# Kernel tuning notes

Hardware: AMD Instinct MI355X
Metric: run time of the kernel (lower is better)

The kernel has to match this reference:

```python
import jax, jax.numpy as jnp
import numpy as np

MASK_PENALTY = 1e15  # matches the TF module's additive mask constant


def setup_inputs() -> dict:
    key = jax.random.key(0)
    k1, k2, k3, k4, k5 = jax.random.split(key, 5)
    B, S, E, DK, DV = 4, 2048, 1024, 128, 128
    inputs = jax.random.normal(k1, (B, S, E), dtype=jnp.float32)
    mask = jax.random.randint(k2, (B, S, S), 0, 2, dtype=jnp.int32)
    # Dense kernels (glorot-ish scale)
    Wq = jax.random.normal(k3, (E, DK), dtype=jnp.float32) / np.float32(np.sqrt(E))
    Wk = jax.random.normal(k4, (E, DK), dtype=jnp.float32) / np.float32(np.sqrt(E))
    Wv = jax.random.normal(k5, (E, DV), dtype=jnp.float32) / np.float32(np.sqrt(E))
    return {"inputs": inputs, "mask": mask, "Wq": Wq, "Wk": Wk, "Wv": Wv}


def reference(inputs, mask, Wq, Wk, Wv):
    # q, k, v projections (no bias)
    q = jnp.einsum("bse,ed->bsd", inputs, Wq)  # [B,S,DK]
    k = jnp.einsum("bse,ed->bsd", inputs, Wk)  # [B,S,DK]
    v = jnp.einsum("bse,ed->bsd", inputs, Wv)  # [B,S,DV]
    dim_k = Wq.shape[-1]
    scale = jnp.asarray(1.0 / np.sqrt(dim_k), dtype=q.dtype)
    dot_p = jnp.einsum("bqd,bkd->bqk", q, k) * scale  # [B,S,S]
    dot_p = dot_p - MASK_PENALTY * mask.astype(dot_p.dtype)
    softm = jax.nn.softmax(dot_p, axis=-1)
    return jnp.einsum("bqk,bkd->bqd", softm, v)  # [B,S,DV]
```

## Files before the change

### kernel.cpp

```cpp
#include <hip/hip_runtime.h>
#include <stdint.h>


#define SEQ   2048
#define EDIM  1024
#define DDIM  128
#define QSCALE 0.08838834764831845f

typedef unsigned short u16;
typedef unsigned int   u32;
using short8 = __attribute__((ext_vector_type(8))) short;
using f32x4  = __attribute__((ext_vector_type(4))) float;
using int4v  = __attribute__((ext_vector_type(4))) int;

__device__ __forceinline__ u16 f2bf(float x) {
    uint32_t u = __float_as_uint(x);
    return (u16)((u + 0x7fffu + ((u >> 16) & 1u)) >> 16);
}

__device__ __forceinline__ void gld16(const void* gsrc, void* lds_dst) {
    __builtin_amdgcn_global_load_lds(
        (const __attribute__((address_space(1))) uint32_t*)(uintptr_t)gsrc,
        (__attribute__((address_space(3))) uint32_t*)(uint32_t)(uintptr_t)lds_dst,
        16, 0, 0);
}

__global__ __launch_bounds__(256) void prep_kernel(
    const int* __restrict__ mask,
    const float* __restrict__ Wq, const float* __restrict__ Wk, const float* __restrict__ Wv,
    u32* __restrict__ Mbits, u16* __restrict__ Wt)
{
    __shared__ u32 nib32[2048];
    __shared__ u16 tl[64][65];
    const int bx = blockIdx.x;
    const int tid = threadIdx.x;
    if (bx < 2048) {
        const int* src = mask + (size_t)bx * 8192;
#pragma unroll
        for (int it = 0; it < 8; ++it) {
            const int idx = it * 256 + tid;
            const int4v v = *(const int4v*)(src + idx * 4);
            const u32 nb = (v[0] != 0 ? 1u : 0u) | (v[1] != 0 ? 2u : 0u)
                         | (v[2] != 0 ? 4u : 0u) | (v[3] != 0 ? 8u : 0u);
            nib32[(idx & 7) * 256 + ((idx >> 3) ^ ((idx & 7) << 2))] = nb;
        }
        __syncthreads();
        u32 word = 0;
#pragma unroll
        for (int j = 0; j < 8; ++j)
            word |= (nib32[j * 256 + (tid ^ (j << 2))] & 0xFu) << (4 * j);
        Mbits[bx * 256 + tid] = word;
    } else {
        const int t = bx - 2048;
        const int wsel = t >> 5;
        const int tile = t & 31;
        const int k0 = (tile >> 1) * 64;
        const int n0 = (tile & 1) * 64;
        const float* W = (wsel == 0) ? Wq : ((wsel == 1) ? Wk : Wv);
#pragma unroll
        for (int it = 0; it < 16; ++it) {
            const int idx = it * 256 + tid;
            const int r = idx >> 6, c = idx & 63;
            tl[c][r] = f2bf(W[(size_t)(k0 + r) * DDIM + n0 + c]);
        }
        __syncthreads();
        u16* Wtp = Wt + (size_t)wsel * DDIM * EDIM;
#pragma unroll
        for (int it = 0; it < 16; ++it) {
            const int idx = it * 256 + tid;
            const int r = idx >> 6, c = idx & 63;
            Wtp[(size_t)(n0 + r) * EDIM + k0 + c] = tl[r][c];
        }
    }
}

__global__ __launch_bounds__(256, 3) void proj_kernel(
    const float* __restrict__ Ain, const u16* __restrict__ Wtb,
    u16* __restrict__ Qb, u16* __restrict__ Kb, u16* __restrict__ Vtb)
{
    __shared__ __align__(16) uint8_t smem[20480];
    const int tid = threadIdx.x;
    const int w = tid >> 6, lane = tid & 63;
    const int lq = lane & 15, lg = lane >> 4;

    const int bid = blockIdx.x;
    const int wg = (bid & 7) * 96 + (bid >> 3);
    const int wm = wg % 3;
    const int m0 = (wg / 3) * 32;
    const u16* Wt = Wtb + (size_t)wm * DDIM * EDIM;

    f32x4 acc[2][2] = {};

#pragma unroll 1
    for (int kt = 0; kt < 16; ++kt) {
        const int k0 = kt * 64;
#pragma unroll
        for (int i = 0; i < 4; ++i) {
            const int G = i * 256 + tid;
            const int n = G >> 3, c = G & 7;
            gld16(Wt + (size_t)n * EDIM + k0 + ((c ^ (n & 7)) << 3),
                  smem + 4096 + i * 4096 + w * 1024);
        }
        {
            const int row = tid >> 3, c = tid & 7;
            const float* s2 = Ain + (size_t)(m0 + row) * EDIM + k0 + ((c ^ (row & 7)) << 3);
            const f32x4 a0 = *(const f32x4*)s2;
            const f32x4 a1 = *(const f32x4*)(s2 + 4);
            short8 v;
            v[0] = (short)f2bf(a0[0]); v[1] = (short)f2bf(a0[1]);
            v[2] = (short)f2bf(a0[2]); v[3] = (short)f2bf(a0[3]);
            v[4] = (short)f2bf(a1[0]); v[5] = (short)f2bf(a1[1]);
            v[6] = (short)f2bf(a1[2]); v[7] = (short)f2bf(a1[3]);
            *(short8*)(smem + row * 128 + (c << 4)) = v;
        }
        __syncthreads();
#pragma unroll
        for (int ks = 0; ks < 2; ++ks) {
            short8 af[2], bfv[2];
#pragma unroll
            for (int mf = 0; mf < 2; ++mf) {
                const int arow = mf * 16 + lq;
                af[mf] = *(const short8*)(smem + arow * 128 + ((((ks << 2) + lg) ^ (arow & 7)) << 4));
            }
#pragma unroll
            for (int nf = 0; nf < 2; ++nf) {
                const int brow = w * 32 + nf * 16 + lq;
                bfv[nf] = *(const short8*)(smem + 4096 + brow * 128 + ((((ks << 2) + lg) ^ (brow & 7)) << 4));
            }
#pragma unroll
            for (int mf = 0; mf < 2; ++mf)
#pragma unroll
                for (int nf = 0; nf < 2; ++nf)
                    acc[mf][nf] = __builtin_amdgcn_mfma_f32_16x16x32_bf16(af[mf], bfv[nf], acc[mf][nf], 0, 0, 0);
        }
        __syncthreads();
    }

    const float osc = (wm == 0) ? QSCALE : 1.0f;
    if (wm < 2) {
#pragma unroll
        for (int mf = 0; mf < 2; ++mf)
#pragma unroll
            for (int nf = 0; nf < 2; ++nf)
#pragma unroll
                for (int rr = 0; rr < 4; ++rr) {
                    const int row = mf * 16 + lg * 4 + rr;
                    const int col = w * 32 + nf * 16 + lq;
                    *(u16*)(smem + row * 256 + (((col >> 3) ^ (row & 7)) << 4) + ((col & 7) << 1))
                        = f2bf(acc[mf][nf][rr] * osc);
                }
        __syncthreads();
        u16* dst = (wm == 0 ? Qb : Kb) + (size_t)m0 * 128;
#pragma unroll
        for (int i = 0; i < 2; ++i) {
            const int j = i * 256 + tid;
            const int row = j >> 4, c = j & 15;
            *(short8*)(dst + (size_t)row * 128 + c * 8)
                = *(const short8*)(smem + row * 256 + ((c ^ (row & 7)) << 4));
        }
    } else {
#pragma unroll
        for (int mf = 0; mf < 2; ++mf)
#pragma unroll
            for (int nf = 0; nf < 2; ++nf)
#pragma unroll
                for (int rr = 0; rr < 4; ++rr) {
                    const int sl = mf * 16 + lg * 4 + rr;
                    const int d  = w * 32 + nf * 16 + lq;
                    *(u16*)(smem + d * 64 + (((sl >> 3) ^ (d & 3)) << 4) + ((sl & 7) << 1))
                        = f2bf(acc[mf][nf][rr]);
                }
        __syncthreads();
        const int b = m0 >> 11, s0b = m0 & 2047;
        u16* dst = Vtb + (size_t)b * DDIM * SEQ;
#pragma unroll
        for (int i = 0; i < 2; ++i) {
            const int j = i * 256 + tid;
            const int dd = j >> 2, c = j & 3;
            *(short8*)(dst + (size_t)dd * SEQ + s0b + c * 8)
                = *(const short8*)(smem + dd * 64 + ((c ^ (dd & 3)) << 4));
        }
    }
}

__global__ __launch_bounds__(512, 1) void flash_kernel(
    const u32* __restrict__ Mb,
    const u16* __restrict__ Qb, const u16* __restrict__ Kb, const u16* __restrict__ Vtb,
    float* __restrict__ out)
{
    __shared__ __align__(16) uint8_t smem[139264];
    __shared__ float ml_m[2][4][16], ml_l[2][4][16], recipL[32];

    const int tid = threadIdx.x;
    const int w = tid >> 6, lane = tid & 63;
    const int qi = w >> 2, ki = w & 3;
    const int lq = lane & 15, lg = lane >> 4;

    const int bid = blockIdx.x;
    const int qt = (bid & 7) * 32 + (bid >> 3);
    const int b = qt >> 6;
    const int q0 = (qt & 63) << 5;
    const size_t qrow0 = (size_t)b * SEQ + q0;

    const u16* Qp = Qb + (qrow0 + qi * 16) * 128;
    const u16* Kp = Kb + (size_t)b * SEQ * 128;
    const u16* Vp = Vtb + (size_t)b * DDIM * SEQ;
    const u32* mrp = Mb + (qrow0 + qi * 16 + lq) * 64 + ki * 16;

    short8 qf[4];
#pragma unroll
    for (int ks = 0; ks < 4; ++ks)
        qf[ks] = *(const short8*)(Qp + (size_t)lq * 128 + ks * 32 + lg * 8);

    f32x4 acc[8] = {};
    float m = -1e30f, l = 0.0f;

    uint8_t* kvb0 = smem + ki * 32768;
    uint8_t* pbase = smem + 131072 + w * 1024;

    auto stage = [&](uint8_t* kvb, int kv0) {
        if (qi == 0) {
#pragma unroll
            for (int i = 0; i < 8; ++i) {
                const int G = i * 64 + lane;
                const int row = G >> 4, c = G & 15;
                gld16(Kp + (size_t)(kv0 + row) * 128 + ((c ^ (row & 7)) << 3),
                      kvb + i * 1024);
            }
        } else {
#pragma unroll
            for (int i = 0; i < 8; ++i) {
                const int G = i * 64 + lane;
                const int dd = G >> 2, c = G & 3;
                gld16(Vp + (size_t)dd * SEQ + kv0 + ((c ^ ((dd ^ (dd >> 2)) & 3)) << 3),
                      kvb + 8192 + i * 1024);
            }
        }
    };

    stage(kvb0, ki * 512);
    u32 mw = mrp[0];
    asm volatile("s_waitcnt vmcnt(0)" ::: "memory");
    __builtin_amdgcn_s_barrier();

#pragma unroll 1
    for (int t = 0; t < 16; ++t) {
        uint8_t* kvb = kvb0 + (t & 1) * 16384;
        if (t < 15) stage(kvb0 + ((t + 1) & 1) * 16384, ki * 512 + (t + 1) * 32);
        const u32 mwn = mrp[(t < 15) ? t + 1 : 15];
        __builtin_amdgcn_sched_barrier(0);

        f32x4 sacc[2] = {};
        __builtin_amdgcn_s_setprio(1);
#pragma unroll
        for (int ks = 0; ks < 4; ++ks)
#pragma unroll
            for (int nf = 0; nf < 2; ++nf) {
                const int krow = nf * 16 + lq;
                const short8 kf = *(const short8*)(kvb + krow * 256 + ((((ks << 2) + lg) ^ (krow & 7)) << 4));
                sacc[nf] = __builtin_amdgcn_mfma_f32_16x16x32_bf16(kf, qf[ks], sacc[nf], 0, 0, 0);
            }
        __builtin_amdgcn_s_setprio(0);

        float sv[2][4];
#pragma unroll
        for (int nf = 0; nf < 2; ++nf)
#pragma unroll
            for (int r = 0; r < 4; ++r)
                sv[nf][r] = sacc[nf][r] + (((mw >> (nf * 16 + lg * 4 + r)) & 1u) ? -1e15f : 0.0f);
        float tm = sv[0][0];
#pragma unroll
        for (int nf = 0; nf < 2; ++nf)
#pragma unroll
            for (int r = 0; r < 4; ++r) tm = fmaxf(tm, sv[nf][r]);
        tm = fmaxf(tm, __shfl_xor(tm, 16));
        tm = fmaxf(tm, __shfl_xor(tm, 32));
        if (!__all(tm <= m + 8.0f)) {
            const float mnew = fmaxf(m, tm);
            const float sf = __expf(m - mnew);
            m = mnew;
            l *= sf;
#pragma unroll
            for (int df = 0; df < 8; ++df) acc[df] *= sf;
        }
        float p[2][4];
        float rs = 0.0f;
#pragma unroll
        for (int nf = 0; nf < 2; ++nf)
#pragma unroll
            for (int r = 0; r < 4; ++r) { p[nf][r] = __expf(sv[nf][r] - m); rs += p[nf][r]; }
        rs += __shfl_xor(rs, 16);
        rs += __shfl_xor(rs, 32);
        l += rs;
        mw = mwn;

#pragma unroll
        for (int nf = 0; nf < 2; ++nf)
#pragma unroll
            for (int h = 0; h < 2; ++h) {
                u32 pk;
                asm("v_cvt_pk_bf16_f32 %0, %1, %2" : "=v"(pk) : "v"(p[nf][2 * h]), "v"(p[nf][2 * h + 1]));
                const int kv = nf * 16 + lg * 4 + 2 * h;
                *(u32*)(pbase + lq * 64 + (((kv >> 3) ^ (lq & 3)) << 4) + ((kv << 1) & 15)) = pk;
            }
        const short8 pf = *(const short8*)(pbase + lq * 64 + ((lg ^ (lq & 3)) << 4));

        __builtin_amdgcn_s_setprio(1);
#pragma unroll
        for (int df = 0; df < 8; ++df) {
            const int dd = df * 16 + lq;
            const short8 vf = *(const short8*)(kvb + 8192 + dd * 64 + ((lg ^ ((dd ^ (dd >> 2)) & 3)) << 4));
            acc[df] = __builtin_amdgcn_mfma_f32_16x16x32_bf16(vf, pf, acc[df], 0, 0, 0);
        }
        __builtin_amdgcn_s_setprio(0);

        asm volatile("s_waitcnt vmcnt(0)" ::: "memory");
        __builtin_amdgcn_s_barrier();
    }

    if (lg == 0) { ml_m[qi][ki][lq] = m; ml_l[qi][ki][lq] = l; }
    __syncthreads();
    {
        const float m0v = ml_m[qi][0][lq], m1v = ml_m[qi][1][lq];
        const float m2v = ml_m[qi][2][lq], m3v = ml_m[qi][3][lq];
        const float mm = fmaxf(fmaxf(m0v, m1v), fmaxf(m2v, m3v));
        const float Lg = ml_l[qi][0][lq] * __expf(m0v - mm) + ml_l[qi][1][lq] * __expf(m1v - mm)
                       + ml_l[qi][2][lq] * __expf(m2v - mm) + ml_l[qi][3][lq] * __expf(m3v - mm);
        if (ki == 0 && lg == 0) recipL[qi * 16 + lq] = 1.0f / Lg;
        const float s = __expf(m - mm);
        float* Ol = (float*)smem;
        float* dstq = Ol + ((size_t)(qi * 4 + ki) * 16 + lq) * 132;
#pragma unroll
        for (int df = 0; df < 8; ++df) {
            const f32x4 vsc = acc[df] * s;
            *(f32x4*)(dstq + df * 16 + lg * 4) = vsc;
        }
    }
    __syncthreads();
    {
        const float* Ol = (const float*)smem;
        const int row = tid >> 4, c0 = (tid & 15) * 8;
        const int rqi = row >> 4, rq = row & 15;
        const float rl = recipL[row];
        f32x4 s0 = {}, s1 = {};
#pragma unroll
        for (int kk = 0; kk < 4; ++kk) {
            const float* p2 = Ol + ((size_t)(rqi * 4 + kk) * 16 + rq) * 132 + c0;
            s0 += *(const f32x4*)p2;
            s1 += *(const f32x4*)(p2 + 4);
        }
        s0 *= rl; s1 *= rl;
        float* op = out + (qrow0 + row) * 128 + c0;
        *(f32x4*)op = s0;
        *(f32x4*)(op + 4) = s1;
    }
}

extern "C" void kernel_launch(void* const* d_in, const int* in_sizes, int n_in,
                              void* d_out, int out_size, void* d_ws, size_t ws_size,
                              hipStream_t stream) {
    (void)in_sizes; (void)n_in; (void)out_size; (void)ws_size;
    const float* inputs = (const float*)d_in[0];
    const int*   mask   = (const int*)d_in[1];
    const float* Wq     = (const float*)d_in[2];
    const float* Wk     = (const float*)d_in[3];
    const float* Wv     = (const float*)d_in[4];
    float* out = (float*)d_out;

    uint8_t* ws = (uint8_t*)d_ws;
    u16* Wtb   = (u16*)ws;
    u16* Qb    = (u16*)(ws + 786432);
    u16* Kb    = (u16*)(ws + 2883584);
    u16* Vtb   = (u16*)(ws + 4980736);
    u32* Mbits = (u32*)(ws + 7077888);

    hipLaunchKernelGGL(prep_kernel, dim3(2144), dim3(256), 0, stream, mask, Wq, Wk, Wv, Mbits, Wtb);
    hipLaunchKernelGGL(proj_kernel, dim3(768), dim3(256), 0, stream, inputs, Wtb, Qb, Kb, Vtb);
    hipLaunchKernelGGL(flash_kernel, dim3(256), dim3(512), 0, stream, Mbits, Qb, Kb, Vtb, out);
}
```

Measured before the change: 170.3 us.

## Fuse mask bitpacking into flash kernel, merge QKV projection, use exp2

Mask bit-packing moves out of the prep kernel and into the flash kernel, which reads its own int32 mask rows into LDS bits. This removes a separate pass that wrote and then re-read a packed mask. The projection kernel now computes Q, K and V together in one 512-thread block per 32 rows with double-buffered LDS staging, so the input tile is loaded once instead of three times. Softmax switches to raw v_exp_f32 with log2e folded into the Q scale, and the rescale threshold is raised. Risks include mask-load latency at the start of the flash kernel and the higher skip threshold affecting precision.

```diff
diff --git a/kernel.cpp b/kernel.cpp
--- a/kernel.cpp
+++ b/kernel.cpp
@@ -5,17 +5,21 @@
 #define SEQ   2048
 #define EDIM  1024
 #define DDIM  128
-#define QSCALE 0.08838834764831845f
+#define QS2   0.1275174329f
 
 typedef unsigned short u16;
 typedef unsigned int   u32;
 using short8 = __attribute__((ext_vector_type(8))) short;
 using f32x4  = __attribute__((ext_vector_type(4))) float;
 using int4v  = __attribute__((ext_vector_type(4))) int;
+using u32x2  = __attribute__((ext_vector_type(2))) unsigned int;
 
 __device__ __forceinline__ u16 f2bf(float x) {
     uint32_t u = __float_as_uint(x);
     return (u16)((u + 0x7fffu + ((u >> 16) & 1u)) >> 16);
+}
+__device__ __forceinline__ float ex2(float x) {
+    float r; asm("v_exp_f32 %0, %1" : "=v"(r) : "v"(x)); return r;
 }
 
 __device__ __forceinline__ void gld16(const void* gsrc, void* lds_dst) {
@@ -26,169 +30,136 @@
 }
 
 __global__ __launch_bounds__(256) void prep_kernel(
-    const int* __restrict__ mask,
     const float* __restrict__ Wq, const float* __restrict__ Wk, const float* __restrict__ Wv,
-    u32* __restrict__ Mbits, u16* __restrict__ Wt)
+    u16* __restrict__ Wt)
 {
-    __shared__ u32 nib32[2048];
     __shared__ u16 tl[64][65];
-    const int bx = blockIdx.x;
+    const int t = blockIdx.x;
     const int tid = threadIdx.x;
-    if (bx < 2048) {
-        const int* src = mask + (size_t)bx * 8192;
-#pragma unroll
-        for (int it = 0; it < 8; ++it) {
-            const int idx = it * 256 + tid;
-            const int4v v = *(const int4v*)(src + idx * 4);
-            const u32 nb = (v[0] != 0 ? 1u : 0u) | (v[1] != 0 ? 2u : 0u)
-                         | (v[2] != 0 ? 4u : 0u) | (v[3] != 0 ? 8u : 0u);
-            nib32[(idx & 7) * 256 + ((idx >> 3) ^ ((idx & 7) << 2))] = nb;
-        }
-        __syncthreads();
-        u32 word = 0;
-#pragma unroll
-        for (int j = 0; j < 8; ++j)
-            word |= (nib32[j * 256 + (tid ^ (j << 2))] & 0xFu) << (4 * j);
-        Mbits[bx * 256 + tid] = word;
-    } else {
-        const int t = bx - 2048;
-        const int wsel = t >> 5;
-        const int tile = t & 31;
-        const int k0 = (tile >> 1) * 64;
-        const int n0 = (tile & 1) * 64;
-        const float* W = (wsel == 0) ? Wq : ((wsel == 1) ? Wk : Wv);
-#pragma unroll
-        for (int it = 0; it < 16; ++it) {
-            const int idx = it * 256 + tid;
-            const int r = idx >> 6, c = idx & 63;
-            tl[c][r] = f2bf(W[(size_t)(k0 + r) * DDIM + n0 + c]);
-        }
-        __syncthreads();
-        u16* Wtp = Wt + (size_t)wsel * DDIM * EDIM;
-#pragma unroll
-        for (int it = 0; it < 16; ++it) {
-            const int idx = it * 256 + tid;
-            const int r = idx >> 6, c = idx & 63;
-            Wtp[(size_t)(n0 + r) * EDIM + k0 + c] = tl[r][c];
-        }
-    }
-}
-
-__global__ __launch_bounds__(256, 3) void proj_kernel(
+    const int wsel = t >> 5;
+    const int tile = t & 31;
+    const int k0 = (tile >> 1) * 64;
+    const int n0 = (tile & 1) * 64;
+    const float* W = (wsel == 0) ? Wq : ((wsel == 1) ? Wk : Wv);
+#pragma unroll
+    for (int it = 0; it < 16; ++it) {
+        const int idx = it * 256 + tid;
+        const int r = idx >> 6, c = idx & 63;
+        tl[c][r] = f2bf(W[(size_t)(k0 + r) * DDIM + n0 + c]);
+    }
+    __syncthreads();
+    u16* Wtp = Wt + (size_t)wsel * DDIM * EDIM;
+#pragma unroll
+    for (int it = 0; it < 16; ++it) {
+        const int idx = it * 256 + tid;
+        const int r = idx >> 6, c = idx & 63;
+        Wtp[(size_t)(n0 + r) * EDIM + k0 + c] = tl[r][c];
+    }
+}
+
+__global__ __launch_bounds__(512, 1) void proj_kernel(
     const float* __restrict__ Ain, const u16* __restrict__ Wtb,
     u16* __restrict__ Qb, u16* __restrict__ Kb, u16* __restrict__ Vtb)
 {
-    __shared__ __align__(16) uint8_t smem[20480];
+    __shared__ __align__(16) uint8_t smem[106496];
     const int tid = threadIdx.x;
     const int w = tid >> 6, lane = tid & 63;
     const int lq = lane & 15, lg = lane >> 4;
 
     const int bid = blockIdx.x;
-    const int wg = (bid & 7) * 96 + (bid >> 3);
-    const int wm = wg % 3;
-    const int m0 = (wg / 3) * 32;
-    const u16* Wt = Wtb + (size_t)wm * DDIM * EDIM;
-
-    f32x4 acc[2][2] = {};
+    const int wg = (bid & 7) * 32 + (bid >> 3);
+    const int m0 = wg * 32;
+
+    f32x4 acc[2][3] = {};
+
+    auto stageP = [&](int buf, int kt) {
+        const int k0 = kt * 64;
+        uint8_t* wtb = smem + 8192 + buf * 49152;
+#pragma unroll
+        for (int i = 0; i < 6; ++i) {
+            const int G = i * 512 + tid;
+            const int n = G >> 3, c = G & 7;
+            gld16(Wtb + (size_t)n * EDIM + k0 + ((c ^ (n & 7)) << 3),
+                  wtb + i * 8192 + w * 1024);
+        }
+        const int row = tid >> 4, c4 = tid & 15;
+        const int c2 = c4 >> 1, h = c4 & 1;
+        const float* s2 = Ain + (size_t)(m0 + row) * EDIM + k0 + c2 * 8 + h * 4;
+        const f32x4 a0 = *(const f32x4*)s2;
+        u32x2 pk;
+        pk[0] = (u32)f2bf(a0[0]) | ((u32)f2bf(a0[1]) << 16);
+        pk[1] = (u32)f2bf(a0[2]) | ((u32)f2bf(a0[3]) << 16);
+        *(u32x2*)(smem + buf * 4096 + row * 128 + ((c2 ^ (row & 7)) << 4) + h * 8) = pk;
+    };
+
+    stageP(0, 0);
+    __syncthreads();
 
 #pragma unroll 1
     for (int kt = 0; kt < 16; ++kt) {
-        const int k0 = kt * 64;
-#pragma unroll
-        for (int i = 0; i < 4; ++i) {
-            const int G = i * 256 + tid;
-            const int n = G >> 3, c = G & 7;
-            gld16(Wt + (size_t)n * EDIM + k0 + ((c ^ (n & 7)) << 3),
-                  smem + 4096 + i * 4096 + w * 1024);
-        }
-        {
-            const int row = tid >> 3, c = tid & 7;
-            const float* s2 = Ain + (size_t)(m0 + row) * EDIM + k0 + ((c ^ (row & 7)) << 3);
-            const f32x4 a0 = *(const f32x4*)s2;
-            const f32x4 a1 = *(const f32x4*)(s2 + 4);
-            short8 v;
-            v[0] = (short)f2bf(a0[0]); v[1] = (short)f2bf(a0[1]);
-            v[2] = (short)f2bf(a0[2]); v[3] = (short)f2bf(a0[3]);
-            v[4] = (short)f2bf(a1[0]); v[5] = (short)f2bf(a1[1]);
-            v[6] = (short)f2bf(a1[2]); v[7] = (short)f2bf(a1[3]);
-            *(short8*)(smem + row * 128 + (c << 4)) = v;
-        }
-        __syncthreads();
+        const int cur = kt & 1;
+        if (kt < 15) stageP(cur ^ 1, kt + 1);
+        const uint8_t* abase = smem + cur * 4096;
+        const uint8_t* wbase = smem + 8192 + cur * 49152;
+        __builtin_amdgcn_s_setprio(1);
 #pragma unroll
         for (int ks = 0; ks < 2; ++ks) {
-            short8 af[2], bfv[2];
+            short8 af[2];
 #pragma unroll
             for (int mf = 0; mf < 2; ++mf) {
                 const int arow = mf * 16 + lq;
-                af[mf] = *(const short8*)(smem + arow * 128 + ((((ks << 2) + lg) ^ (arow & 7)) << 4));
-            }
-#pragma unroll
-            for (int nf = 0; nf < 2; ++nf) {
-                const int brow = w * 32 + nf * 16 + lq;
-                bfv[nf] = *(const short8*)(smem + 4096 + brow * 128 + ((((ks << 2) + lg) ^ (brow & 7)) << 4));
-            }
-#pragma unroll
-            for (int mf = 0; mf < 2; ++mf)
-#pragma unroll
-                for (int nf = 0; nf < 2; ++nf)
-                    acc[mf][nf] = __builtin_amdgcn_mfma_f32_16x16x32_bf16(af[mf], bfv[nf], acc[mf][nf], 0, 0, 0);
-        }
+                af[mf] = *(const short8*)(abase + arow * 128 + ((((ks << 2) + lg) ^ (arow & 7)) << 4));
+            }
+#pragma unroll
+            for (int j = 0; j < 3; ++j) {
+                const int brow = (w + j * 8) * 16 + lq;
+                const short8 bf = *(const short8*)(wbase + brow * 128 + ((((ks << 2) + lg) ^ (brow & 7)) << 4));
+#pragma unroll
+                for (int mf = 0; mf < 2; ++mf)
+                    acc[mf][j] = __builtin_amdgcn_mfma_f32_16x16x32_bf16(af[mf], bf, acc[mf][j], 0, 0, 0);
+            }
+        }
+        __builtin_amdgcn_s_setprio(0);
         __syncthreads();
     }
 
-    const float osc = (wm == 0) ? QSCALE : 1.0f;
-    if (wm < 2) {
-#pragma unroll
-        for (int mf = 0; mf < 2; ++mf)
-#pragma unroll
-            for (int nf = 0; nf < 2; ++nf)
-#pragma unroll
-                for (int rr = 0; rr < 4; ++rr) {
-                    const int row = mf * 16 + lg * 4 + rr;
-                    const int col = w * 32 + nf * 16 + lq;
-                    *(u16*)(smem + row * 256 + (((col >> 3) ^ (row & 7)) << 4) + ((col & 7) << 1))
-                        = f2bf(acc[mf][nf][rr] * osc);
-                }
-        __syncthreads();
-        u16* dst = (wm == 0 ? Qb : Kb) + (size_t)m0 * 128;
-#pragma unroll
-        for (int i = 0; i < 2; ++i) {
-            const int j = i * 256 + tid;
-            const int row = j >> 4, c = j & 15;
-            *(short8*)(dst + (size_t)row * 128 + c * 8)
-                = *(const short8*)(smem + row * 256 + ((c ^ (row & 7)) << 4));
-        }
-    } else {
-#pragma unroll
-        for (int mf = 0; mf < 2; ++mf)
-#pragma unroll
-            for (int nf = 0; nf < 2; ++nf)
-#pragma unroll
-                for (int rr = 0; rr < 4; ++rr) {
-                    const int sl = mf * 16 + lg * 4 + rr;
-                    const int d  = w * 32 + nf * 16 + lq;
-                    *(u16*)(smem + d * 64 + (((sl >> 3) ^ (d & 3)) << 4) + ((sl & 7) << 1))
-                        = f2bf(acc[mf][nf][rr]);
-                }
-        __syncthreads();
+#pragma unroll
+    for (int mf = 0; mf < 2; ++mf)
+#pragma unroll
+        for (int r = 0; r < 4; ++r) {
+            const int mrow = mf * 16 + lg * 4 + r;
+            const int n = w * 16 + lq;
+            *(u16*)(smem + mrow * 256 + (((n >> 3) ^ (mrow & 7)) << 4) + ((n & 7) << 1))
+                = f2bf(acc[mf][0][r] * QS2);
+            *(u16*)(smem + 8192 + mrow * 256 + (((n >> 3) ^ (mrow & 7)) << 4) + ((n & 7) << 1))
+                = f2bf(acc[mf][1][r]);
+            const int d = n, s = mrow;
+            *(u16*)(smem + 16384 + d * 64 + (((s >> 3) ^ (d & 3)) << 4) + ((s & 7) << 1))
+                = f2bf(acc[mf][2][r]);
+        }
+    __syncthreads();
+    {
         const int b = m0 >> 11, s0b = m0 & 2047;
-        u16* dst = Vtb + (size_t)b * DDIM * SEQ;
-#pragma unroll
-        for (int i = 0; i < 2; ++i) {
-            const int j = i * 256 + tid;
-            const int dd = j >> 2, c = j & 3;
-            *(short8*)(dst + (size_t)dd * SEQ + s0b + c * 8)
-                = *(const short8*)(smem + dd * 64 + ((c ^ (dd & 3)) << 4));
-        }
+        const int mm2 = tid >> 4, gp = tid & 15;
+        const int n0 = (gp ^ (mm2 & 7)) * 8;
+        const short8 vq = *(const short8*)(smem + mm2 * 256 + (gp << 4));
+        *(short8*)(Qb + (size_t)(m0 + mm2) * 128 + n0) = vq;
+        const short8 vk = *(const short8*)(smem + 8192 + mm2 * 256 + (gp << 4));
+        *(short8*)(Kb + (size_t)(m0 + mm2) * 128 + n0) = vk;
+        const int d = tid >> 2, cg = tid & 3;
+        const int sg = cg ^ (d & 3);
+        const short8 vv = *(const short8*)(smem + 16384 + d * 64 + (cg << 4));
+        *(short8*)(Vtb + (size_t)b * DDIM * SEQ + (size_t)d * SEQ + s0b + sg * 8) = vv;
     }
 }
 
 __global__ __launch_bounds__(512, 1) void flash_kernel(
-    const u32* __restrict__ Mb,
+    const int* __restrict__ mask,
     const u16* __restrict__ Qb, const u16* __restrict__ Kb, const u16* __restrict__ Vtb,
     float* __restrict__ out)
 {
     __shared__ __align__(16) uint8_t smem[139264];
+    __shared__ u32 mlds[2112];
     __shared__ float ml_m[2][4][16], ml_l[2][4][16], recipL[32];
 
     const int tid = threadIdx.x;
@@ -205,15 +176,6 @@
     const u16* Qp = Qb + (qrow0 + qi * 16) * 128;
     const u16* Kp = Kb + (size_t)b * SEQ * 128;
     const u16* Vp = Vtb + (size_t)b * DDIM * SEQ;
-    const u32* mrp = Mb + (qrow0 + qi * 16 + lq) * 64 + ki * 16;
-
-    short8 qf[4];
-#pragma unroll
-    for (int ks = 0; ks < 4; ++ks)
-        qf[ks] = *(const short8*)(Qp + (size_t)lq * 128 + ks * 32 + lg * 8);
-
-    f32x4 acc[8] = {};
-    float m = -1e30f, l = 0.0f;
 
     uint8_t* kvb0 = smem + ki * 32768;
     uint8_t* pbase = smem + 131072 + w * 1024;
@@ -239,15 +201,38 @@
     };
 
     stage(kvb0, ki * 512);
-    u32 mw = mrp[0];
-    asm volatile("s_waitcnt vmcnt(0)" ::: "memory");
-    __builtin_amdgcn_s_barrier();
+    short8 qf[4];
+#pragma unroll
+    for (int ks = 0; ks < 4; ++ks)
+        qf[ks] = *(const short8*)(Qp + (size_t)lq * 128 + ks * 32 + lg * 8);
+    {
+        const int r = tid >> 4, c0 = (tid & 15) * 4;
+        const int* srcm = mask + (qrow0 + r) * (size_t)SEQ + (size_t)c0 * 32;
+#pragma unroll
+        for (int j = 0; j < 4; ++j) {
+            u32 bits = 0;
+#pragma unroll
+            for (int it = 0; it < 8; ++it) {
+                const int4v v = *(const int4v*)(srcm + j * 32 + it * 4);
+                bits |= (v[0] != 0 ? 1u : 0u) << (it * 4 + 0);
+                bits |= (v[1] != 0 ? 1u : 0u) << (it * 4 + 1);
+                bits |= (v[2] != 0 ? 1u : 0u) << (it * 4 + 2);
+                bits |= (v[3] != 0 ? 1u : 0u) << (it * 4 + 3);
+            }
+            mlds[r * 66 + c0 + j] = bits;
+        }
+    }
+    __syncthreads();
+
+    f32x4 acc[8] = {};
+    float m = -1e30f, l = 0.0f;
+    const int mbidx = (qi * 16 + lq) * 66 + ki * 16;
 
 #pragma unroll 1
     for (int t = 0; t < 16; ++t) {
         uint8_t* kvb = kvb0 + (t & 1) * 16384;
         if (t < 15) stage(kvb0 + ((t + 1) & 1) * 16384, ki * 512 + (t + 1) * 32);
-        const u32 mwn = mrp[(t < 15) ? t + 1 : 15];
+        const u32 mw = mlds[mbidx + t];
         __builtin_amdgcn_sched_barrier(0);
 
         f32x4 sacc[2] = {};
@@ -275,9 +260,9 @@
             for (int r = 0; r < 4; ++r) tm = fmaxf(tm, sv[nf][r]);
         tm = fmaxf(tm, __shfl_xor(tm, 16));
         tm = fmaxf(tm, __shfl_xor(tm, 32));
-        if (!__all(tm <= m + 8.0f)) {
+        if (!__all(tm <= m + 13.0f)) {
             const float mnew = fmaxf(m, tm);
-            const float sf = __expf(m - mnew);
+            const float sf = ex2(m - mnew);
             m = mnew;
             l *= sf;
 #pragma unroll
@@ -288,11 +273,10 @@
 #pragma unroll
         for (int nf = 0; nf < 2; ++nf)
 #pragma unroll
-            for (int r = 0; r < 4; ++r) { p[nf][r] = __expf(sv[nf][r] - m); rs += p[nf][r]; }
+            for (int r = 0; r < 4; ++r) { p[nf][r] = ex2(sv[nf][r] - m); rs += p[nf][r]; }
         rs += __shfl_xor(rs, 16);
         rs += __shfl_xor(rs, 32);
         l += rs;
-        mw = mwn;
 
 #pragma unroll
         for (int nf = 0; nf < 2; ++nf)
@@ -324,10 +308,10 @@
         const float m0v = ml_m[qi][0][lq], m1v = ml_m[qi][1][lq];
         const float m2v = ml_m[qi][2][lq], m3v = ml_m[qi][3][lq];
         const float mm = fmaxf(fmaxf(m0v, m1v), fmaxf(m2v, m3v));
-        const float Lg = ml_l[qi][0][lq] * __expf(m0v - mm) + ml_l[qi][1][lq] * __expf(m1v - mm)
-                       + ml_l[qi][2][lq] * __expf(m2v - mm) + ml_l[qi][3][lq] * __expf(m3v - mm);
+        const float Lg = ml_l[qi][0][lq] * ex2(m0v - mm) + ml_l[qi][1][lq] * ex2(m1v - mm)
+                       + ml_l[qi][2][lq] * ex2(m2v - mm) + ml_l[qi][3][lq] * ex2(m3v - mm);
         if (ki == 0 && lg == 0) recipL[qi * 16 + lq] = 1.0f / Lg;
-        const float s = __expf(m - mm);
+        const float s = ex2(m - mm);
         float* Ol = (float*)smem;
         float* dstq = Ol + ((size_t)(qi * 4 + ki) * 16 + lq) * 132;
 #pragma unroll
@@ -368,13 +352,12 @@
     float* out = (float*)d_out;
 
     uint8_t* ws = (uint8_t*)d_ws;
-    u16* Wtb   = (u16*)ws;
-    u16* Qb    = (u16*)(ws + 786432);
-    u16* Kb    = (u16*)(ws + 2883584);
-    u16* Vtb   = (u16*)(ws + 4980736);
-    u32* Mbits = (u32*)(ws + 7077888);
-
-    hipLaunchKernelGGL(prep_kernel, dim3(2144), dim3(256), 0, stream, mask, Wq, Wk, Wv, Mbits, Wtb);
-    hipLaunchKernelGGL(proj_kernel, dim3(768), dim3(256), 0, stream, inputs, Wtb, Qb, Kb, Vtb);
-    hipLaunchKernelGGL(flash_kernel, dim3(256), dim3(512), 0, stream, Mbits, Qb, Kb, Vtb, out);
-}
+    u16* Wtb = (u16*)ws;
+    u16* Qb  = (u16*)(ws + 786432);
+    u16* Kb  = (u16*)(ws + 2883584);
+    u16* Vtb = (u16*)(ws + 4980736);
+
+    hipLaunchKernelGGL(prep_kernel, dim3(96), dim3(256), 0, stream, Wq, Wk, Wv, Wtb);
+    hipLaunchKernelGGL(proj_kernel, dim3(256), dim3(512), 0, stream, inputs, Wtb, Qb, Kb, Vtb);
+    hipLaunchKernelGGL(flash_kernel, dim3(256), dim3(512), 0, stream, mask, Qb, Kb, Vtb, out);
+}
```

Result: slower. 174.8 us (+2.7%).
